# Kernel tuning notes

Hardware: AMD Instinct MI355X
Metric: run time of the kernel (lower is better)

## Reference

```python
import jax, jax.numpy as jnp
import numpy as np

IN_CH = 8      # in_channels
CIN = 80       # cin_channels (mel)
DI_BASE = 2
POS_GROUP = 4
NCH = 256      # n_channels
NLAYERS = 8
K = 3          # kernel_size
B = 1          # spect batch; audio batch = B * POS_GROUP
T = 4096
C2L = 2 * NCH * NLAYERS


def _conv1x1(x, w, b):
    # x: [B, C, T], w: [O, C], b: [O]
    return jnp.einsum('bct,oc->bot', x, w) + b[None, :, None]


def _dilated_conv(x, w, b, dilation):
    # x: [B, C, T], w: [O, C, K], 'same' padding as in torch Conv1d
    pad = dilation * (K - 1) // 2
    y = jax.lax.conv_general_dilated(
        x, w, window_strides=(1,), padding=[(pad, pad)],
        rhs_dilation=(dilation,), dimension_numbers=('NCH', 'OIH', 'NCH'))
    return y + b[None, :, None]


def setup_inputs() -> dict:
    key = jax.random.key(0)
    ks = jax.random.split(key, 12)
    s = 0.05
    d = {}
    d['audio'] = jax.random.normal(ks[0], (B * POS_GROUP, IN_CH, T), jnp.float32)
    d['spect'] = jax.random.normal(ks[1], (B, CIN, T), jnp.float32)
    d['pos'] = jax.random.randint(ks[2], (B * POS_GROUP,), 0, POS_GROUP)
    d['start_w'] = jax.random.normal(ks[3], (NCH, IN_CH), jnp.float32) * s
    d['start_b'] = jnp.zeros((NCH,), jnp.float32)
    d['cond_w'] = jax.random.normal(ks[4], (C2L, CIN), jnp.float32) * s
    d['cond_b'] = jnp.zeros((C2L,), jnp.float32)
    d['pos_emb_w'] = jax.random.normal(ks[5], (POS_GROUP, 128), jnp.float32) * s
    d['pos_lin_w'] = jax.random.normal(ks[6], (C2L, 128), jnp.float32) * s
    d['pos_lin_b'] = jnp.zeros((C2L,), jnp.float32)
    d['in_w'] = jax.random.normal(ks[7], (NLAYERS, 2 * NCH, NCH, K), jnp.float32) * s
    d['in_b'] = jnp.zeros((NLAYERS, 2 * NCH), jnp.float32)
    d['rs_w'] = jax.random.normal(ks[8], (NLAYERS - 1, 2 * NCH, NCH), jnp.float32) * s
    d['rs_b'] = jnp.zeros((NLAYERS - 1, 2 * NCH), jnp.float32)
    d['rs_last_w'] = jax.random.normal(ks[9], (NCH, NCH), jnp.float32) * s
    d['rs_last_b'] = jnp.zeros((NCH,), jnp.float32)
    d['end_w'] = jax.random.normal(ks[10], (2 * IN_CH, NCH), jnp.float32) * s
    d['end_b'] = jnp.zeros((2 * IN_CH,), jnp.float32)
    return d


def reference(audio, spect, pos, start_w, start_b, cond_w, cond_b,
              pos_emb_w, pos_lin_w, pos_lin_b, in_w, in_b,
              rs_w, rs_b, rs_last_w, rs_last_b, end_w, end_b):
    h = _conv1x1(audio, start_w, start_b)               # [BG, NCH, T]
    out = jnp.zeros_like(h)
    cond = _conv1x1(spect, cond_w, cond_b)              # [B, 2*NCH*L, T]
    # repeat(1, pos_group, 1).view(-1, C, T) == consecutive batch tiling
    cond = jnp.repeat(cond, POS_GROUP, axis=0)          # [BG, 2*NCH*L, T]
    pe = jax.nn.relu(pos_emb_w[pos])                    # [BG, 128]
    pc = (pe @ pos_lin_w.T + pos_lin_b)[:, :, None]     # [BG, 2*NCH*L, 1]
    for i in range(NLAYERS):
        off = i * 2 * NCH
        in_act = (_dilated_conv(h, in_w[i], in_b[i], DI_BASE ** i)
                  + cond[:, off:off + 2 * NCH]
                  + pc[:, off:off + 2 * NCH])
        acts = jnp.tanh(in_act[:, :NCH]) * jax.nn.sigmoid(in_act[:, NCH:])
        if i < NLAYERS - 1:
            rs = _conv1x1(acts, rs_w[i], rs_b[i])       # [BG, 2*NCH, T]
            h = h + rs[:, :NCH]
            out = out + rs[:, NCH:]
        else:
            out = out + _conv1x1(acts, rs_last_w, rs_last_b)
    y = _conv1x1(out, end_w, end_b)                     # [BG, 2*IN_CH, T]
    return y[:, :IN_CH], y[:, IN_CH:]
```

## Files before the change

### kernel.cpp

```cpp
#include <hip/hip_runtime.h>
#include <stdint.h>

#define T_LEN 4096
#define PAD   128
#define HROWS (T_LEN + 2*PAD)
#define NCH   256
#define M2    512
#define BG    4
#define NL    8

using f4  = __attribute__((ext_vector_type(4))) float;
using bh8 = __attribute__((ext_vector_type(8))) short;
using s4v = __attribute__((ext_vector_type(4))) short;
using u4  = __attribute__((ext_vector_type(4))) unsigned int;

static __device__ __forceinline__ short f2b(float f){
  unsigned u = __builtin_bit_cast(unsigned, f);
  unsigned r = (u + 0x7FFFu + ((u >> 16) & 1u)) >> 16;
  return (short)r;
}
static __device__ __forceinline__ float b2f(short s){
  unsigned u = ((unsigned)(unsigned short)s) << 16;
  return __builtin_bit_cast(float, u);
}

#define MFMA(a,b,c) __builtin_amdgcn_mfma_f32_16x16x32_bf16((a),(b),(c),0,0,0)


#define PAD_BLK0 1024
#define E_BLK0   1280
#define ST_BLK0  1408
#define CB_BLK0  1536
#define H0_BLK0  1600
#define ALL_BLKS 1856

__global__ __launch_bounds__(256) void prep_all(
    const float* __restrict__ audio, const float* __restrict__ spect,
    const int* __restrict__ pos, const float* __restrict__ start_w,
    const float* __restrict__ start_b, const float* __restrict__ cond_w,
    const float* __restrict__ cond_b, const float* __restrict__ pos_emb_w,
    const float* __restrict__ pos_lin_w, const float* __restrict__ pos_lin_b,
    const float* __restrict__ in_w, const float* __restrict__ in_b,
    const float* __restrict__ rs_w, const float* __restrict__ rs_b,
    const float* __restrict__ rs_last_w, const float* __restrict__ rs_last_b,
    const float* __restrict__ end_w, const float* __restrict__ end_b,
    short* __restrict__ W1, short* __restrict__ W2, short* __restrict__ Wcn,
    float* __restrict__ rsb8, short* __restrict__ hA, short* __restrict__ hB,
    short* __restrict__ Es, float* __restrict__ ebl, short* __restrict__ spectT,
    float* __restrict__ cb){
  __shared__ float smem[4224];
  const int bid = blockIdx.x, tid = threadIdx.x;

  if (bid < PAD_BLK0){
    const int G1 = NL*3*8*8*4*64;
    const int G2 = NL*8*8*2*64;
    const int G4 = NL*8*4*4*64;
    const int n3 = NL*M2;
    for (int q = bid*256 + tid; q < G1+G2+G4+n3; q += 1024*256){
      if (q < G1){
        int lane = q & 63, f = (q >> 6) & 3, kk = (q >> 8) & 7, w = (q >> 11) & 7;
        int lt = q >> 14;
        int tap = lt % 3, l = lt / 3;
        int o = (f < 2) ? (w*32 + f*16 + (lane & 15)) : (256 + w*32 + (f-2)*16 + (lane & 15));
        int c0 = kk*32 + (lane >> 4)*8;
        const float* src = in_w + (((size_t)(l*M2 + o)*NCH + c0)*3) + tap;
        bh8 pk;
        #pragma unroll
        for (int j = 0; j < 8; ++j) pk[j] = f2b(src[j*3]);
        *(bh8*)(W1 + (size_t)q*8) = pk;
      } else if (q < G1+G2){
        int p = q - G1;
        int lane = p & 63, f = (p >> 6) & 1, kk = (p >> 7) & 7, w = (p >> 10) & 7;
        int l = p >> 13;
        int o = w*32 + f*16 + (lane & 15);
        int c0 = kk*32 + (lane >> 4)*8;
        bh8 pk;
        if (l < 7){
          const f4* s = (const f4*)(rs_w + ((size_t)(l*M2 + o))*NCH + c0);
          f4 a = s[0], bvv = s[1];
          #pragma unroll
          for (int j = 0; j < 4; ++j){ pk[j] = f2b(a[j]); pk[4+j] = f2b(bvv[j]); }
        } else {
          #pragma unroll
          for (int j = 0; j < 8; ++j) pk[j] = 0;
        }
        *(bh8*)(W2 + (size_t)p*8) = pk;
      } else if (q < G1+G2+G4){
        int p = q - G1 - G2;
        int lane = p & 63, f = (p >> 6) & 3, kk = (p >> 8) & 3, w = (p >> 10) & 7;
        int l = p >> 13;
        int o = (f < 2) ? (w*32 + f*16 + (lane & 15)) : (256 + w*32 + (f-2)*16 + (lane & 15));
        int k0 = kk*32 + (lane >> 4)*8;
        bh8 pk;
        if (k0 < 80){
          const f4* s = (const f4*)(cond_w + (size_t)(l*M2 + o)*80 + k0);
          f4 a = s[0], bvv = s[1];
          #pragma unroll
          for (int j = 0; j < 4; ++j){ pk[j] = f2b(a[j]); pk[4+j] = f2b(bvv[j]); }
        } else {
          #pragma unroll
          for (int j = 0; j < 8; ++j) pk[j] = 0;
        }
        *(bh8*)(Wcn + (size_t)p*8) = pk;
      } else {
        int k = q - G1 - G2 - G4;
        int o = k & 511, l = k >> 9;
        rsb8[k] = (l < 7) ? rs_b[l*M2 + o] : 0.f;
      }
    }
  } else if (bid < E_BLK0){
    int i = (bid - PAD_BLK0)*256 + tid;
    short* h = (i < 32768) ? hA : hB;
    int j = (i & 32767) << 3;
    int b = j >> 16;
    int r = j & 65535;
    int row = r >> 8, c = r & 255;
    int grow = (row < PAD) ? row : (T_LEN + PAD + (row - PAD));
    *(u4*)(h + ((size_t)b*HROWS + grow)*NCH + c) = (u4){0,0,0,0};
  } else if (bid < ST_BLK0){
    float* ew_s = smem; float* red = smem + 256;
    int e = bid - E_BLK0;
    const int l = e >> 4, o = e & 15;
    const int c = tid;
    ew_s[c] = end_w[o*256 + c];
    __syncthreads();
    const float* Wsrc = (l < 7) ? (rs_w + ((size_t)(l*M2 + NCH))*NCH) : rs_last_w;
    float acc = 0.f;
    #pragma unroll 8
    for (int cp = 0; cp < 256; ++cp)
      acc += ew_s[cp] * Wsrc[(size_t)cp*NCH + c];
    int kk = c >> 5, g = (c >> 3) & 3, j = c & 7;
    Es[(((size_t)l*8 + kk)*64 + g*16 + o)*8 + j] = f2b(acc);
    float bv = (l < 7) ? rs_b[l*M2 + NCH + c] : rs_last_b[c];
    red[c] = ew_s[c] * bv;
    __syncthreads();
    for (int s = 128; s > 0; s >>= 1){
      if (c < s) red[c] += red[c + s];
      __syncthreads();
    }
    if (c == 0) ebl[l*16 + o] = red[0] + ((l == 0) ? end_b[o] : 0.f);
  } else if (bid < CB_BLK0){
    float (*tile)[65] = (float(*)[65])smem;
    int e = bid - ST_BLK0;
    int t0 = (e & 63)*64, k0 = (e >> 6)*64;
    for (int i = tid; i < 64*64; i += 256){
      int kr = i >> 6, tt = i & 63;
      int k = k0 + kr;
      tile[kr][tt] = (k < 80) ? spect[(size_t)k*T_LEN + t0 + tt] : 0.f;
    }
    __syncthreads();
    for (int i = tid; i < 64*64; i += 256){
      int r = i >> 6, kk = i & 63;
      spectT[(size_t)(t0 + r)*128 + k0 + kk] = f2b(tile[kk][r]);
    }
  } else if (bid < H0_BLK0){
    int e = bid - CB_BLK0;
    int b = e >> 4;
    int ch = (e & 15)*256 + tid;
    int p = pos[b];
    float acc = pos_lin_b[ch] + in_b[ch] + cond_b[ch];
    for (int k = 0; k < 128; ++k){
      float ev = pos_emb_w[p*128 + k];
      ev = ev > 0.f ? ev : 0.f;
      acc += ev * pos_lin_w[ch*128 + k];
    }
    cb[b*4096 + ch] = acc;
  } else {
    float* sw = smem; float* sb = smem + 2048;
    int e = bid - H0_BLK0;
    int b = e >> 6, t0 = (e & 63)*64;
    for (int i = tid; i < NCH*8; i += 256) sw[i] = start_w[i];
    for (int i = tid; i < NCH;   i += 256) sb[i] = start_b[i];
    __syncthreads();
    int t = t0 + (tid & 63);
    int cg = tid >> 6;
    float av[8];
    #pragma unroll
    for (int ic = 0; ic < 8; ++ic) av[ic] = audio[((size_t)(b*8 + ic))*T_LEN + t];
    short* dst = hA + ((size_t)b*HROWS + PAD + t)*NCH;
    for (int c = cg*64; c < cg*64 + 64; ++c){
      float acc = sb[c];
      #pragma unroll
      for (int ic = 0; ic < 8; ++ic) acc += sw[c*8 + ic]*av[ic];
      dst[c] = f2b(acc);
    }
  }
}

__global__ __launch_bounds__(512, 2) void wn_layer(
    const short* __restrict__ hSrc, short* __restrict__ hDst,
    const short* __restrict__ W1l, const short* __restrict__ W2l,
    const short* __restrict__ Wcl, const short* __restrict__ Esl,
    const short* __restrict__ spectTp,
    const float* __restrict__ cb_l, const float* __restrict__ rsb_l,
    const float* __restrict__ ebl_l, float* __restrict__ yacc,
    int dil, int flags){

  __shared__ short Ht[192*NCH];
  __shared__ short xb[64*NCH];
  __shared__ short St[64*128];

  const int tid  = threadIdx.x;
  const int w    = tid >> 6, lane = tid & 63;
  const int l15  = lane & 15, g = lane >> 4;
  const int lin  = blockIdx.x + (blockIdx.y << 6);
  const int nl2  = ((lin & 7) << 5) + (lin >> 3);
  const int tile = nl2 & 63, b = nl2 >> 6;
  const int sw8  = (l15 & 7) << 3;
  const bool first = flags & 1, last = flags & 2;
  const int tbR  = (dil <= 64) ? dil : 64;

  f4 acc[4][4];
  #pragma unroll
  for (int f = 0; f < 4; ++f)
    #pragma unroll
    for (int nf = 0; nf < 4; ++nf) acc[f][nf] = (f4){0.f,0.f,0.f,0.f};

  bh8 Ap[3][4], Bp[3][4];

#define LAc(S, BUF) do{ const short* _p = Wcl + w*8192 + (S)*2048 + lane*8; \
    Ap[BUF][0]=*(const bh8*)(_p);      Ap[BUF][1]=*(const bh8*)(_p+512); \
    Ap[BUF][2]=*(const bh8*)(_p+1024); Ap[BUF][3]=*(const bh8*)(_p+1536); }while(0)
#define LBc(S, BUF) do{ const int _c=((S)*32+g*8)^sw8; \
    Bp[BUF][0]=*(const bh8*)(St + ( 0+l15)*128 + _c); \
    Bp[BUF][1]=*(const bh8*)(St + (16+l15)*128 + _c); \
    Bp[BUF][2]=*(const bh8*)(St + (32+l15)*128 + _c); \
    Bp[BUF][3]=*(const bh8*)(St + (48+l15)*128 + _c); }while(0)
#define LA1(S, BUF) do{ const int _tap=(S)>>3, _kk=(S)&7; \
    const short* _p = W1l + _tap*131072 + w*16384 + _kk*2048 + lane*8; \
    Ap[BUF][0]=*(const bh8*)(_p);      Ap[BUF][1]=*(const bh8*)(_p+512); \
    Ap[BUF][2]=*(const bh8*)(_p+1024); Ap[BUF][3]=*(const bh8*)(_p+1536); }while(0)
#define LB1(S, BUF) do{ const int _tap=(S)>>3, _kk=(S)&7; \
    const int _tb=_tap*tbR; const int _sw=(((_tb+l15)&7)<<3); \
    const short* _hb = Ht + (_tb+l15)*NCH + ((_kk*32+g*8)^_sw); \
    Bp[BUF][0]=*(const bh8*)(_hb); \
    Bp[BUF][1]=*(const bh8*)(_hb + 16*NCH); \
    Bp[BUF][2]=*(const bh8*)(_hb + 32*NCH); \
    Bp[BUF][3]=*(const bh8*)(_hb + 48*NCH); }while(0)
#define LAX(S, BUF) do{ if((S)<3) LAc((S),BUF); else LA1((S)-3,BUF); }while(0)
#define LBX(S, BUF) do{ if((S)<3) LBc((S),BUF); else LB1((S)-3,BUF); }while(0)
#define LA2(S, BUF) do{ \
    const short* _p = W2l + w*8192 + (S)*1024 + lane*8; \
    Ap[BUF][0]=*(const bh8*)(_p);      Ap[BUF][1]=*(const bh8*)(_p+512); }while(0)
#define LB2(S, BUF) do{ const int _c=((S)*32+g*8)^sw8; \
    Bp[BUF][0]=*(const bh8*)(xb + ( 0+l15)*NCH + _c); \
    Bp[BUF][1]=*(const bh8*)(xb + (16+l15)*NCH + _c); \
    Bp[BUF][2]=*(const bh8*)(xb + (32+l15)*NCH + _c); \
    Bp[BUF][3]=*(const bh8*)(xb + (48+l15)*NCH + _c); }while(0)

  LAX(0, 0);

  {
    const int nrows32 = ((dil <= 64) ? (64 + 2*dil) : 192) * 32;
    for (int i = tid; i < nrows32; i += 512){
      int r = i >> 5, c16 = (i & 31) << 3;
      int grow = (dil <= 64) ? (tile*64 - dil + r)
                             : (tile*64 + ((r >> 6) - 1)*128 + (r & 63));
      u4 v = *(const u4*)(hSrc + ((size_t)(b*HROWS + PAD + grow))*NCH + c16);
      *(u4*)(Ht + r*NCH + (c16 ^ ((r & 7) << 3))) = v;
    }
    #pragma unroll
    for (int s = 0; s < 2; ++s){
      int id = tid + s*512;
      int r = id >> 4, c8 = (id & 15) << 3;
      u4 v = *(const u4*)(spectTp + (size_t)(tile*64 + r)*128 + c8);
      *(u4*)(St + r*128 + (c8 ^ ((r & 7) << 3))) = v;
    }
  }
  __syncthreads();

  LBX(0, 0);
  LAX(1, 1); LBX(1, 1);
  #pragma unroll
  for (int s = 0; s < 27; ++s){
    const int cur = s % 3, pf = (s+2) % 3;
    if (s < 25){ LAX(s+2, pf); LBX(s+2, pf); }
    #pragma unroll
    for (int f = 0; f < 4; ++f)
      #pragma unroll
      for (int nf = 0; nf < 4; ++nf)
        acc[f][nf] = MFMA(Ap[cur][f], Bp[cur][nf], acc[f][nf]);
  }

  float bias[4][4];
  #pragma unroll
  for (int f = 0; f < 4; ++f){
    int ch = ((f < 2) ? (w*32 + f*16) : (256 + w*32 + (f-2)*16)) + 4*g;
    f4 t = *(const f4*)(cb_l + b*4096 + ch);
    #pragma unroll
    for (int j = 0; j < 4; ++j) bias[f][j] = t[j];
  }
  float rbv[2][4];
  #pragma unroll
  for (int f = 0; f < 2; ++f){
    f4 t = *(const f4*)(rsb_l + w*32 + f*16 + 4*g);
    #pragma unroll
    for (int j = 0; j < 4; ++j) rbv[f][j] = t[j];
  }

  #pragma unroll
  for (int f = 0; f < 2; ++f){
    #pragma unroll
    for (int nf = 0; nf < 4; ++nf){
      int tl = nf*16 + l15;
      s4v pk;
      #pragma unroll
      for (int j = 0; j < 4; ++j){
        float xl = acc[f][nf][j]   + bias[f][j];
        float xh = acc[f+2][nf][j] + bias[f+2][j];
        xl = fminf(fmaxf(xl, -30.f), 30.f);
        xh = fminf(fmaxf(xh, -30.f), 30.f);
        float e2 = __expf(2.f*xl);
        float th = (e2 - 1.f)/(e2 + 1.f);
        float sg = 1.f/(1.f + __expf(-xh));
        pk[j] = f2b(th * sg);
      }
      *(s4v*)(xb + tl*NCH + ((w*32 + f*16 + 4*g) ^ sw8)) = pk;
    }
  }
  if (!last) LA2(0, 0);
  __syncthreads();

  if (!last){
    #pragma unroll
    for (int f = 0; f < 2; ++f)
      #pragma unroll
      for (int nf = 0; nf < 4; ++nf) acc[f][nf] = (f4){0.f,0.f,0.f,0.f};
    LB2(0, 0);
    #pragma unroll
    for (int s = 0; s < 8; ++s){
      const int cur = s & 1, nxt = cur ^ 1;
      if (s < 7){ LA2(s+1, nxt); LB2(s+1, nxt); }
      #pragma unroll
      for (int f = 0; f < 2; ++f)
        #pragma unroll
        for (int nf = 0; nf < 4; ++nf)
          acc[f][nf] = MFMA(Ap[cur][f], Bp[cur][nf], acc[f][nf]);
    }
    const int swc = (((tbR + l15) & 7) << 3);
    #pragma unroll
    for (int f = 0; f < 2; ++f){
      #pragma unroll
      for (int nf = 0; nf < 4; ++nf){
        int tl = nf*16 + l15;
        int cb0 = w*32 + f*16 + 4*g;
        s4v hold = *(const s4v*)(Ht + (tbR + tl)*NCH + (cb0 ^ swc));
        s4v pk;
        #pragma unroll
        for (int j = 0; j < 4; ++j)
          pk[j] = f2b(b2f(hold[j]) + acc[f][nf][j] + rbv[f][j]);
        *(s4v*)(hDst + ((size_t)b*HROWS + PAD + tile*64 + tl)*NCH + cb0) = pk;
      }
    }
  }
  {
    const int nfq = w & 3, kh = w >> 2;
    f4 ya = (f4){0.f,0.f,0.f,0.f};
    #pragma unroll
    for (int s = 0; s < 4; ++s){
      int kks = kh*4 + s;
      bh8 av = *(const bh8*)(Esl + ((size_t)kks*64 + lane)*8);
      bh8 bv = *(const bh8*)(xb + (nfq*16 + l15)*NCH + ((kks*32 + g*8) ^ sw8));
      ya = MFMA(av, bv, ya);
    }
    float* yp = yacc + (((size_t)(b*T_LEN + tile*64 + nfq*16 + l15))*2 + kh)*16 + g*4;
    f4 prev = first ? (f4){0.f,0.f,0.f,0.f} : *(const f4*)yp;
    f4 o;
    #pragma unroll
    for (int j = 0; j < 4; ++j)
      o[j] = prev[j] + ya[j] + ((kh == 0) ? ebl_l[g*4 + j] : 0.f);
    *(f4*)yp = o;
  }
#undef LAc
#undef LBc
#undef LA1
#undef LB1
#undef LAX
#undef LBX
#undef LA2
#undef LB2
}

__global__ void final_y(const float* __restrict__ yacc, float* __restrict__ y){
  __shared__ float tl[16][65];
  int b = blockIdx.y, t0 = blockIdx.x*64;
  int i = threadIdx.x;
  #pragma unroll
  for (int s = 0; s < 4; ++s){
    int idx = i + s*256;
    int t = idx >> 4, o = idx & 15;
    size_t base = ((size_t)(b*T_LEN + t0 + t))*32 + o;
    tl[o][t] = yacc[base] + yacc[base + 16];
  }
  __syncthreads();
  #pragma unroll
  for (int s = 0; s < 4; ++s){
    int idx = i + s*256;
    int o = idx >> 6, t = idx & 63;
    float v = tl[o][t];
    float* dst = (o < 8) ? (y + ((size_t)(b*8 + o))*T_LEN)
                         : (y + 131072 + ((size_t)(b*8 + o - 8))*T_LEN);
    dst[t0 + t] = v;
  }
}

extern "C" void kernel_launch(void* const* d_in, const int* in_sizes, int n_in,
                              void* d_out, int out_size, void* d_ws, size_t ws_size,
                              hipStream_t stream){
  const float* audio      = (const float*)d_in[0];
  const float* spect      = (const float*)d_in[1];
  const int*   pos        = (const int*)  d_in[2];
  const float* start_w    = (const float*)d_in[3];
  const float* start_b    = (const float*)d_in[4];
  const float* cond_w     = (const float*)d_in[5];
  const float* cond_b     = (const float*)d_in[6];
  const float* pos_emb_w  = (const float*)d_in[7];
  const float* pos_lin_w  = (const float*)d_in[8];
  const float* pos_lin_b  = (const float*)d_in[9];
  const float* in_w       = (const float*)d_in[10];
  const float* in_b       = (const float*)d_in[11];
  const float* rs_w       = (const float*)d_in[12];
  const float* rs_b       = (const float*)d_in[13];
  const float* rs_last_w  = (const float*)d_in[14];
  const float* rs_last_b  = (const float*)d_in[15];
  const float* end_w      = (const float*)d_in[16];
  const float* end_b      = (const float*)d_in[17];
  float* y = (float*)d_out;

  char* ws = (char*)d_ws;
  size_t off = 0;
  auto alloc = [&](size_t bytes) -> void* {
    void* p = ws + off;
    off += (bytes + 255) & ~(size_t)255;
    return p;
  };
  const size_t hBytes = (size_t)BG*HROWS*NCH*2;
  short* hA     = (short*)alloc(hBytes);
  short* hB     = (short*)alloc(hBytes);
  short* W1     = (short*)alloc((size_t)NL*3*8*8*4*512*2);
  short* W2     = (short*)alloc((size_t)NL*8*8*2*512*2);
  short* Wcn    = (short*)alloc((size_t)NL*8*4*4*512*2);
  float* rsb8   = (float*)alloc((size_t)NL*M2*4);
  float* cb     = (float*)alloc((size_t)BG*4096*4);
  short* spectT = (short*)alloc((size_t)4096*128*2);
  short* Es     = (short*)alloc((size_t)NL*8*64*8*2);
  float* ebl    = (float*)alloc((size_t)NL*16*4);
  float* yacc   = (float*)alloc((size_t)BG*T_LEN*2*16*4);
  if (off > ws_size) return;

  prep_all<<<ALL_BLKS, 256, 0, stream>>>(
      audio, spect, pos, start_w, start_b, cond_w, cond_b, pos_emb_w, pos_lin_w,
      pos_lin_b, in_w, in_b, rs_w, rs_b, rs_last_w, rs_last_b, end_w, end_b,
      W1, W2, Wcn, rsb8, hA, hB, Es, ebl, spectT, cb);

  for (int l = 0; l < NL; ++l){
    const short* hS = (l & 1) ? hB : hA;
    short*       hD = (l & 1) ? hA : hB;
    int flags = (l == 0 ? 1 : 0) | (l == NL-1 ? 2 : 0);
    wn_layer<<<dim3(64, BG), 512, 0, stream>>>(
        hS, hD,
        W1 + (size_t)l*3*131072,
        W2 + (size_t)l*65536,
        Wcn + (size_t)l*65536,
        Es + (size_t)l*4096,
        spectT,
        cb + l*M2,
        rsb8 + l*M2,
        ebl + l*16,
        yacc, 1 << l, flags);
  }
  final_y<<<dim3(64, BG), 256, 0, stream>>>(yacc, y);
}
```

Baseline: 220.2 us.

## Fuse all WaveNet layers and final output into one cooperative persistent kernel

Replaces the eight per-layer launches and the final transpose kernel with a single cooperative kernel that loops over layers and uses a grid-wide barrier between them. The final output transpose reuses shared memory inside the same kernel. The goal is to remove per-launch overhead and the tail and ramp gaps between layer kernels. In exchange it adds grid.sync cost and requires all 256 blocks to be co-resident. The restrict qualifiers are also dropped, which may weaken compiler optimisations.

```diff
diff --git a/kernel.cpp b/kernel.cpp
--- a/kernel.cpp
+++ b/kernel.cpp
@@ -1,5 +1,8 @@
 #include <hip/hip_runtime.h>
+#include <hip/hip_cooperative_groups.h>
 #include <stdint.h>
+
+namespace cg = cooperative_groups;
 
 #define T_LEN 4096
 #define PAD   128
@@ -187,36 +190,47 @@
   }
 }
 
-__global__ __launch_bounds__(512, 2) void wn_layer(
-    const short* __restrict__ hSrc, short* __restrict__ hDst,
-    const short* __restrict__ W1l, const short* __restrict__ W2l,
-    const short* __restrict__ Wcl, const short* __restrict__ Esl,
-    const short* __restrict__ spectTp,
-    const float* __restrict__ cb_l, const float* __restrict__ rsb_l,
-    const float* __restrict__ ebl_l, float* __restrict__ yacc,
-    int dil, int flags){
+__global__ __launch_bounds__(512, 2) void wn_all(
+    short* hA, short* hB, const short* W1, const short* W2, const short* Wcn,
+    const float* rsb8, const float* cb, const short* spectTp, const short* Es,
+    const float* ebl, float* yacc, float* y){
 
   __shared__ short Ht[192*NCH];
   __shared__ short xb[64*NCH];
   __shared__ short St[64*128];
 
+  cg::grid_group grid = cg::this_grid();
+
   const int tid  = threadIdx.x;
   const int w    = tid >> 6, lane = tid & 63;
   const int l15  = lane & 15, g = lane >> 4;
-  const int lin  = blockIdx.x + (blockIdx.y << 6);
+  const int lin  = blockIdx.x;
   const int nl2  = ((lin & 7) << 5) + (lin >> 3);
   const int tile = nl2 & 63, b = nl2 >> 6;
   const int sw8  = (l15 & 7) << 3;
-  const bool first = flags & 1, last = flags & 2;
-  const int tbR  = (dil <= 64) ? dil : 64;
-
-  f4 acc[4][4];
-  #pragma unroll
-  for (int f = 0; f < 4; ++f)
-    #pragma unroll
-    for (int nf = 0; nf < 4; ++nf) acc[f][nf] = (f4){0.f,0.f,0.f,0.f};
-
-  bh8 Ap[3][4], Bp[3][4];
+
+  #pragma unroll 1
+  for (int l = 0; l < NL; ++l){
+    const short* W1l  = W1 + (size_t)l*3*131072;
+    const short* W2l  = W2 + (size_t)l*65536;
+    const short* Wcl  = Wcn + (size_t)l*65536;
+    const short* Esl  = Es + (size_t)l*4096;
+    const float* cb_l = cb + l*M2;
+    const float* rsb_l= rsb8 + l*M2;
+    const float* ebl_l= ebl + l*16;
+    const short* hSrc = (l & 1) ? hB : hA;
+    short*       hDst = (l & 1) ? hA : hB;
+    const int dil  = 1 << l;
+    const bool first = (l == 0), last = (l == NL-1);
+    const int tbR  = (dil <= 64) ? dil : 64;
+
+    f4 acc[4][4];
+    #pragma unroll
+    for (int f = 0; f < 4; ++f)
+      #pragma unroll
+      for (int nf = 0; nf < 4; ++nf) acc[f][nf] = (f4){0.f,0.f,0.f,0.f};
+
+    bh8 Ap[3][4], Bp[3][4];
 
 #define LAc(S, BUF) do{ const short* _p = Wcl + w*8192 + (S)*2048 + lane*8; \
     Ap[BUF][0]=*(const bh8*)(_p);      Ap[BUF][1]=*(const bh8*)(_p+512); \
@@ -248,129 +262,129 @@
     Bp[BUF][2]=*(const bh8*)(xb + (32+l15)*NCH + _c); \
     Bp[BUF][3]=*(const bh8*)(xb + (48+l15)*NCH + _c); }while(0)
 
-  LAX(0, 0);
-
-  {
-    const int nrows32 = ((dil <= 64) ? (64 + 2*dil) : 192) * 32;
-    for (int i = tid; i < nrows32; i += 512){
-      int r = i >> 5, c16 = (i & 31) << 3;
-      int grow = (dil <= 64) ? (tile*64 - dil + r)
-                             : (tile*64 + ((r >> 6) - 1)*128 + (r & 63));
-      u4 v = *(const u4*)(hSrc + ((size_t)(b*HROWS + PAD + grow))*NCH + c16);
-      *(u4*)(Ht + r*NCH + (c16 ^ ((r & 7) << 3))) = v;
-    }
-    #pragma unroll
-    for (int s = 0; s < 2; ++s){
-      int id = tid + s*512;
-      int r = id >> 4, c8 = (id & 15) << 3;
-      u4 v = *(const u4*)(spectTp + (size_t)(tile*64 + r)*128 + c8);
-      *(u4*)(St + r*128 + (c8 ^ ((r & 7) << 3))) = v;
-    }
-  }
-  __syncthreads();
-
-  LBX(0, 0);
-  LAX(1, 1); LBX(1, 1);
-  #pragma unroll
-  for (int s = 0; s < 27; ++s){
-    const int cur = s % 3, pf = (s+2) % 3;
-    if (s < 25){ LAX(s+2, pf); LBX(s+2, pf); }
-    #pragma unroll
-    for (int f = 0; f < 4; ++f)
-      #pragma unroll
-      for (int nf = 0; nf < 4; ++nf)
-        acc[f][nf] = MFMA(Ap[cur][f], Bp[cur][nf], acc[f][nf]);
-  }
-
-  float bias[4][4];
-  #pragma unroll
-  for (int f = 0; f < 4; ++f){
-    int ch = ((f < 2) ? (w*32 + f*16) : (256 + w*32 + (f-2)*16)) + 4*g;
-    f4 t = *(const f4*)(cb_l + b*4096 + ch);
-    #pragma unroll
-    for (int j = 0; j < 4; ++j) bias[f][j] = t[j];
-  }
-  float rbv[2][4];
-  #pragma unroll
-  for (int f = 0; f < 2; ++f){
-    f4 t = *(const f4*)(rsb_l + w*32 + f*16 + 4*g);
-    #pragma unroll
-    for (int j = 0; j < 4; ++j) rbv[f][j] = t[j];
-  }
-
-  #pragma unroll
-  for (int f = 0; f < 2; ++f){
-    #pragma unroll
-    for (int nf = 0; nf < 4; ++nf){
-      int tl = nf*16 + l15;
-      s4v pk;
-      #pragma unroll
-      for (int j = 0; j < 4; ++j){
-        float xl = acc[f][nf][j]   + bias[f][j];
-        float xh = acc[f+2][nf][j] + bias[f+2][j];
-        xl = fminf(fmaxf(xl, -30.f), 30.f);
-        xh = fminf(fmaxf(xh, -30.f), 30.f);
-        float e2 = __expf(2.f*xl);
-        float th = (e2 - 1.f)/(e2 + 1.f);
-        float sg = 1.f/(1.f + __expf(-xh));
-        pk[j] = f2b(th * sg);
-      }
-      *(s4v*)(xb + tl*NCH + ((w*32 + f*16 + 4*g) ^ sw8)) = pk;
-    }
-  }
-  if (!last) LA2(0, 0);
-  __syncthreads();
-
-  if (!last){
-    #pragma unroll
-    for (int f = 0; f < 2; ++f)
-      #pragma unroll
-      for (int nf = 0; nf < 4; ++nf) acc[f][nf] = (f4){0.f,0.f,0.f,0.f};
-    LB2(0, 0);
-    #pragma unroll
-    for (int s = 0; s < 8; ++s){
-      const int cur = s & 1, nxt = cur ^ 1;
-      if (s < 7){ LA2(s+1, nxt); LB2(s+1, nxt); }
-      #pragma unroll
-      for (int f = 0; f < 2; ++f)
+    LAX(0, 0);
+
+    {
+      const int nrows32 = ((dil <= 64) ? (64 + 2*dil) : 192) * 32;
+      for (int i = tid; i < nrows32; i += 512){
+        int r = i >> 5, c16 = (i & 31) << 3;
+        int grow = (dil <= 64) ? (tile*64 - dil + r)
+                               : (tile*64 + ((r >> 6) - 1)*128 + (r & 63));
+        u4 v = *(const u4*)(hSrc + ((size_t)(b*HROWS + PAD + grow))*NCH + c16);
+        *(u4*)(Ht + r*NCH + (c16 ^ ((r & 7) << 3))) = v;
+      }
+      #pragma unroll
+      for (int s = 0; s < 2; ++s){
+        int id = tid + s*512;
+        int r = id >> 4, c8 = (id & 15) << 3;
+        u4 v = *(const u4*)(spectTp + (size_t)(tile*64 + r)*128 + c8);
+        *(u4*)(St + r*128 + (c8 ^ ((r & 7) << 3))) = v;
+      }
+    }
+    __syncthreads();
+
+    LBX(0, 0);
+    LAX(1, 1); LBX(1, 1);
+    #pragma unroll
+    for (int s = 0; s < 27; ++s){
+      const int cur = s % 3, pf = (s+2) % 3;
+      if (s < 25){ LAX(s+2, pf); LBX(s+2, pf); }
+      #pragma unroll
+      for (int f = 0; f < 4; ++f)
         #pragma unroll
         for (int nf = 0; nf < 4; ++nf)
           acc[f][nf] = MFMA(Ap[cur][f], Bp[cur][nf], acc[f][nf]);
     }
-    const int swc = (((tbR + l15) & 7) << 3);
+
+    float bias[4][4];
+    #pragma unroll
+    for (int f = 0; f < 4; ++f){
+      int ch = ((f < 2) ? (w*32 + f*16) : (256 + w*32 + (f-2)*16)) + 4*g;
+      f4 t = *(const f4*)(cb_l + b*4096 + ch);
+      #pragma unroll
+      for (int j = 0; j < 4; ++j) bias[f][j] = t[j];
+    }
+    float rbv[2][4];
+    #pragma unroll
+    for (int f = 0; f < 2; ++f){
+      f4 t = *(const f4*)(rsb_l + w*32 + f*16 + 4*g);
+      #pragma unroll
+      for (int j = 0; j < 4; ++j) rbv[f][j] = t[j];
+    }
+
     #pragma unroll
     for (int f = 0; f < 2; ++f){
       #pragma unroll
       for (int nf = 0; nf < 4; ++nf){
         int tl = nf*16 + l15;
-        int cb0 = w*32 + f*16 + 4*g;
-        s4v hold = *(const s4v*)(Ht + (tbR + tl)*NCH + (cb0 ^ swc));
         s4v pk;
         #pragma unroll
-        for (int j = 0; j < 4; ++j)
-          pk[j] = f2b(b2f(hold[j]) + acc[f][nf][j] + rbv[f][j]);
-        *(s4v*)(hDst + ((size_t)b*HROWS + PAD + tile*64 + tl)*NCH + cb0) = pk;
-      }
-    }
-  }
-  {
-    const int nfq = w & 3, kh = w >> 2;
-    f4 ya = (f4){0.f,0.f,0.f,0.f};
-    #pragma unroll
-    for (int s = 0; s < 4; ++s){
-      int kks = kh*4 + s;
-      bh8 av = *(const bh8*)(Esl + ((size_t)kks*64 + lane)*8);
-      bh8 bv = *(const bh8*)(xb + (nfq*16 + l15)*NCH + ((kks*32 + g*8) ^ sw8));
-      ya = MFMA(av, bv, ya);
-    }
-    float* yp = yacc + (((size_t)(b*T_LEN + tile*64 + nfq*16 + l15))*2 + kh)*16 + g*4;
-    f4 prev = first ? (f4){0.f,0.f,0.f,0.f} : *(const f4*)yp;
-    f4 o;
-    #pragma unroll
-    for (int j = 0; j < 4; ++j)
-      o[j] = prev[j] + ya[j] + ((kh == 0) ? ebl_l[g*4 + j] : 0.f);
-    *(f4*)yp = o;
-  }
+        for (int j = 0; j < 4; ++j){
+          float xl = acc[f][nf][j]   + bias[f][j];
+          float xh = acc[f+2][nf][j] + bias[f+2][j];
+          xl = fminf(fmaxf(xl, -30.f), 30.f);
+          xh = fminf(fmaxf(xh, -30.f), 30.f);
+          float e2 = __expf(2.f*xl);
+          float th = (e2 - 1.f)/(e2 + 1.f);
+          float sg = 1.f/(1.f + __expf(-xh));
+          pk[j] = f2b(th * sg);
+        }
+        *(s4v*)(xb + tl*NCH + ((w*32 + f*16 + 4*g) ^ sw8)) = pk;
+      }
+    }
+    if (!last) LA2(0, 0);
+    __syncthreads();
+
+    if (!last){
+      #pragma unroll
+      for (int f = 0; f < 2; ++f)
+        #pragma unroll
+        for (int nf = 0; nf < 4; ++nf) acc[f][nf] = (f4){0.f,0.f,0.f,0.f};
+      LB2(0, 0);
+      #pragma unroll
+      for (int s = 0; s < 8; ++s){
+        const int cur = s & 1, nxt = cur ^ 1;
+        if (s < 7){ LA2(s+1, nxt); LB2(s+1, nxt); }
+        #pragma unroll
+        for (int f = 0; f < 2; ++f)
+          #pragma unroll
+          for (int nf = 0; nf < 4; ++nf)
+            acc[f][nf] = MFMA(Ap[cur][f], Bp[cur][nf], acc[f][nf]);
+      }
+      const int swc = (((tbR + l15) & 7) << 3);
+      #pragma unroll
+      for (int f = 0; f < 2; ++f){
+        #pragma unroll
+        for (int nf = 0; nf < 4; ++nf){
+          int tl = nf*16 + l15;
+          int cb0 = w*32 + f*16 + 4*g;
+          s4v hold = *(const s4v*)(Ht + (tbR + tl)*NCH + (cb0 ^ swc));
+          s4v pk;
+          #pragma unroll
+          for (int j = 0; j < 4; ++j)
+            pk[j] = f2b(b2f(hold[j]) + acc[f][nf][j] + rbv[f][j]);
+          *(s4v*)(hDst + ((size_t)b*HROWS + PAD + tile*64 + tl)*NCH + cb0) = pk;
+        }
+      }
+    }
+    {
+      const int nfq = w & 3, kh = w >> 2;
+      f4 ya = (f4){0.f,0.f,0.f,0.f};
+      #pragma unroll
+      for (int s = 0; s < 4; ++s){
+        int kks = kh*4 + s;
+        bh8 av = *(const bh8*)(Esl + ((size_t)kks*64 + lane)*8);
+        bh8 bv = *(const bh8*)(xb + (nfq*16 + l15)*NCH + ((kks*32 + g*8) ^ sw8));
+        ya = MFMA(av, bv, ya);
+      }
+      float* yp = yacc + (((size_t)(b*T_LEN + tile*64 + nfq*16 + l15))*2 + kh)*16 + g*4;
+      f4 prev = first ? (f4){0.f,0.f,0.f,0.f} : *(const f4*)yp;
+      f4 o;
+      #pragma unroll
+      for (int j = 0; j < 4; ++j)
+        o[j] = prev[j] + ya[j] + ((kh == 0) ? ebl_l[g*4 + j] : 0.f);
+      *(f4*)yp = o;
+    }
 #undef LAc
 #undef LBc
 #undef LA1
@@ -379,28 +393,34 @@
 #undef LBX
 #undef LA2
 #undef LB2
-}
-
-__global__ void final_y(const float* __restrict__ yacc, float* __restrict__ y){
-  __shared__ float tl[16][65];
-  int b = blockIdx.y, t0 = blockIdx.x*64;
-  int i = threadIdx.x;
-  #pragma unroll
-  for (int s = 0; s < 4; ++s){
-    int idx = i + s*256;
-    int t = idx >> 4, o = idx & 15;
-    size_t base = ((size_t)(b*T_LEN + t0 + t))*32 + o;
-    tl[o][t] = yacc[base] + yacc[base + 16];
+
+    if (l < NL-1){
+      __threadfence();
+      grid.sync();
+    }
   }
+
+  __threadfence_block();
   __syncthreads();
-  #pragma unroll
-  for (int s = 0; s < 4; ++s){
-    int idx = i + s*256;
-    int o = idx >> 6, t = idx & 63;
-    float v = tl[o][t];
-    float* dst = (o < 8) ? (y + ((size_t)(b*8 + o))*T_LEN)
-                         : (y + 131072 + ((size_t)(b*8 + o - 8))*T_LEN);
-    dst[t0 + t] = v;
+  {
+    float* tl = (float*)Ht;
+    #pragma unroll
+    for (int s = 0; s < 2; ++s){
+      int idx = tid + s*512;
+      int t = idx >> 4, o = idx & 15;
+      size_t base = ((size_t)(b*T_LEN + tile*64 + t))*32 + o;
+      tl[o*65 + t] = yacc[base] + yacc[base + 16];
+    }
+    __syncthreads();
+    #pragma unroll
+    for (int s = 0; s < 2; ++s){
+      int idx = tid + s*512;
+      int o = idx >> 6, t = idx & 63;
+      float v = tl[o*65 + t];
+      float* dst = (o < 8) ? (y + ((size_t)(b*8 + o))*T_LEN)
+                           : (y + 131072 + ((size_t)(b*8 + o - 8))*T_LEN);
+      dst[tile*64 + t] = v;
+    }
   }
 }
 
@@ -453,21 +473,8 @@
       pos_lin_b, in_w, in_b, rs_w, rs_b, rs_last_w, rs_last_b, end_w, end_b,
       W1, W2, Wcn, rsb8, hA, hB, Es, ebl, spectT, cb);
 
-  for (int l = 0; l < NL; ++l){
-    const short* hS = (l & 1) ? hB : hA;
-    short*       hD = (l & 1) ? hA : hB;
-    int flags = (l == 0 ? 1 : 0) | (l == NL-1 ? 2 : 0);
-    wn_layer<<<dim3(64, BG), 512, 0, stream>>>(
-        hS, hD,
-        W1 + (size_t)l*3*131072,
-        W2 + (size_t)l*65536,
-        Wcn + (size_t)l*65536,
-        Es + (size_t)l*4096,
-        spectT,
-        cb + l*M2,
-        rsb8 + l*M2,
-        ebl + l*16,
-        yacc, 1 << l, flags);
-  }
-  final_y<<<dim3(64, BG), 256, 0, stream>>>(yacc, y);
+  void* kargs[] = { (void*)&hA, (void*)&hB, (void*)&W1, (void*)&W2, (void*)&Wcn,
+                    (void*)&rsb8, (void*)&cb, (void*)&spectT, (void*)&Es,
+                    (void*)&ebl, (void*)&yacc, (void*)&y };
+  hipLaunchCooperativeKernel((void*)wn_all, dim3(256), dim3(512), kargs, 0, stream);
 }
```

Measured after the change: 781.5 us. 255% more time.
